# Performance work log

Measured on AMD Instinct MI355X. Metric: run time of the kernel, lower is better.

The kernel has to match this reference:

```python
import jax, jax.numpy as jnp
import numpy as np

S, B, V, E, H, L, HM = 256, 16, 20000, 512, 256, 2, 128  # seq, batch, vocab, emb, hidden, layers, mlp hidden
THRESH = 0.5


def setup_inputs() -> dict:
    key = jax.random.key(0)
    ks = jax.random.split(key, 8)
    sc = 0.05
    concepts = jax.random.randint(ks[0], (S, B), 0, V)
    concepts_lengths = jnp.full((B,), S, dtype=jnp.int32)  # full-length sequences
    emb = jax.random.normal(ks[1], (V, E), jnp.float32) * sc
    # stacked PyTorch-style LSTM weights: [layer, direction(0=fwd,1=bwd), 4H, in]
    w_ih = jax.random.normal(ks[2], (L, 2, 4 * H, E), jnp.float32) * sc
    w_hh = jax.random.normal(ks[3], (L, 2, 4 * H, H), jnp.float32) * sc
    b = jax.random.normal(ks[4], (L, 2, 4 * H), jnp.float32) * sc  # b_ih + b_hh combined
    Ua = jax.random.normal(ks[5], (HM, 2 * H), jnp.float32) * sc
    Wa = jax.random.normal(ks[6], (HM, 2 * H), jnp.float32) * sc
    va = jax.random.normal(ks[7], (1, HM), jnp.float32) * sc
    return dict(concepts=concepts, concepts_lengths=concepts_lengths, emb=emb,
                w_ih=w_ih, w_hh=w_hh, b=b, Ua=Ua, Wa=Wa, va=va)


def _lstm_dir(x, wi, wh, bb, reverse):
    # x: [S, B, in]; PyTorch gate order i, f, g, o
    h0 = jnp.zeros((x.shape[1], H), x.dtype)

    def step(carry, xt):
        h, c = carry
        g = xt @ wi.T + h @ wh.T + bb  # [B, 4H]
        i, f, gg, o = jnp.split(g, 4, axis=-1)
        c = jax.nn.sigmoid(f) * c + jax.nn.sigmoid(i) * jnp.tanh(gg)
        h = jax.nn.sigmoid(o) * jnp.tanh(c)
        return (h, c), h

    _, hs = jax.lax.scan(step, (h0, h0), x, reverse=reverse)
    return hs  # [S, B, H]


def reference(concepts, concepts_lengths, emb, w_ih, w_hh, b, Ua, Wa, va):
    x = emb[concepts]  # [S, B, E]
    for l in range(L):  # fixed small layer count
        f = _lstm_dir(x, w_ih[l, 0], w_hh[l, 0], b[l, 0], False)
        r = _lstm_dir(x, w_ih[l, 1], w_hh[l, 1], b[l, 1], True)
        x = jnp.concatenate([f, r], axis=-1)  # [S, B, 2H]
    enc = x.transpose(1, 0, 2)  # [B, S, 2H]
    p = enc @ Ua.T  # [B, S, HM]  Ua(parent)
    c = enc @ Wa.T  # [B, S, HM]  Wa(child)
    # fused pairwise: va(tanh(Ua(p_i) + Wa(c_j))) -> [B, S, S]
    scores = jnp.einsum('bijh,h->bij', jnp.tanh(p[:, :, None, :] + c[:, None, :, :]), va[0])
    predictions = (jax.nn.sigmoid(scores) >= THRESH).astype(jnp.int32)
    return scores, predictions
```

## Files before the change

kernel.cpp:

```cpp
#include <hip/hip_runtime.h>


#define S_    256
#define B_    16
#define E_    512
#define H_    256
#define HM_   128
#define M_    4096

typedef __attribute__((ext_vector_type(8))) short short8;
typedef __attribute__((ext_vector_type(4))) float f32x4;
union u32x4s8 { unsigned int u[4]; uint4 u4; short8 v; };

__device__ __forceinline__ float sigm(float x) { return 1.f / (1.f + __expf(-x)); }
__device__ __forceinline__ float tanh_fast(float x) {
  x = fminf(fmaxf(x, -15.f), 15.f);
  float e = __expf(2.f * x);
  return (e - 1.f) / (e + 1.f);
}
__device__ __forceinline__ unsigned short f2bf(float f) {
  unsigned u = __float_as_uint(f);
  u += 0x7FFFu + ((u >> 16) & 1u);
  return (unsigned short)(u >> 16);
}
__device__ __forceinline__ float bf2f(unsigned short s) {
  return __uint_as_float(((unsigned)s) << 16);
}
__device__ __forceinline__ unsigned int packsplit(float f) {
  unsigned short m = f2bf(f);
  unsigned short r = f2bf(f - bf2f(m));
  return (unsigned)m | ((unsigned)r << 16);
}

__global__ void k_gather_pk(const int* __restrict__ concepts, const float* __restrict__ emb,
                            unsigned int* __restrict__ Xpk) {
  int m = blockIdx.x;
  int tok = concepts[m];
  const float4* src = reinterpret_cast<const float4*>(emb + (size_t)tok * E_);
  uint4* dst = reinterpret_cast<uint4*>(Xpk + (size_t)m * E_);
  for (int i = threadIdx.x; i < E_ / 4; i += blockDim.x) {
    float4 v = src[i];
    uint4 o;
    o.x = packsplit(v.x); o.y = packsplit(v.y); o.z = packsplit(v.z); o.w = packsplit(v.w);
    dst[i] = o;
  }
}

__global__ void k_pack(const float* __restrict__ in, unsigned int* __restrict__ out, int n4) {
  int i = blockIdx.x * blockDim.x + threadIdx.x;
  if (i < n4) {
    float4 v = reinterpret_cast<const float4*>(in)[i];
    uint4 o;
    o.x = packsplit(v.x); o.y = packsplit(v.y); o.z = packsplit(v.z); o.w = packsplit(v.w);
    reinterpret_cast<uint4*>(out)[i] = o;
  }
}

__global__ __launch_bounds__(256) void k_gemm_pk(const unsigned int* __restrict__ Apk,
                                                 const unsigned int* __restrict__ Wpk,
                                                 const float* __restrict__ bias,
                                                 float* __restrict__ C, int N, int K) {
  __shared__ unsigned int As[128][36];
  __shared__ unsigned int Ws2[128][36];
  const int bm = blockIdx.x * 128, bn = blockIdx.y * 128;
  const int tid = threadIdx.x;
  const int wave = tid >> 6, lane = tid & 63;
  const int wm = (wave >> 1) << 6, wn = (wave & 1) << 6;
  const int l16 = lane & 15, quad = lane >> 4;
  const int r = tid >> 1, cb = (tid & 1) << 4;

  f32x4 acc[4][4];
#pragma unroll
  for (int i = 0; i < 4; ++i)
#pragma unroll
    for (int j = 0; j < 4; ++j) acc[i][j] = (f32x4){0.f, 0.f, 0.f, 0.f};

  for (int k0 = 0; k0 < K; k0 += 32) {
    const unsigned int* pa = Apk + (size_t)(bm + r) * K + k0 + cb;
    const unsigned int* pw = Wpk + (size_t)(bn + r) * K + k0 + cb;
    uint4 a0 = *(const uint4*)pa, a1 = *(const uint4*)(pa + 4),
          a2 = *(const uint4*)(pa + 8), a3 = *(const uint4*)(pa + 12);
    uint4 w0 = *(const uint4*)pw, w1 = *(const uint4*)(pw + 4),
          w2 = *(const uint4*)(pw + 8), w3 = *(const uint4*)(pw + 12);
    __syncthreads();
    *(uint4*)&As[r][cb] = a0;  *(uint4*)&As[r][cb + 4] = a1;
    *(uint4*)&As[r][cb + 8] = a2; *(uint4*)&As[r][cb + 12] = a3;
    *(uint4*)&Ws2[r][cb] = w0; *(uint4*)&Ws2[r][cb + 4] = w1;
    *(uint4*)&Ws2[r][cb + 8] = w2; *(uint4*)&Ws2[r][cb + 12] = w3;
    __syncthreads();

    short8 Amv[4], Arv[4], Bmv[4], Brv[4];
#pragma unroll
    for (int t = 0; t < 4; ++t) {
      const unsigned int* p = &As[wm + (t << 4) + l16][quad << 3];
      uint4 p0 = *(const uint4*)p, p1 = *(const uint4*)(p + 4);
      u32x4s8 m, rr;
      m.u[0] = __builtin_amdgcn_perm(p0.y, p0.x, 0x05040100u);
      rr.u[0] = __builtin_amdgcn_perm(p0.y, p0.x, 0x07060302u);
      m.u[1] = __builtin_amdgcn_perm(p0.w, p0.z, 0x05040100u);
      rr.u[1] = __builtin_amdgcn_perm(p0.w, p0.z, 0x07060302u);
      m.u[2] = __builtin_amdgcn_perm(p1.y, p1.x, 0x05040100u);
      rr.u[2] = __builtin_amdgcn_perm(p1.y, p1.x, 0x07060302u);
      m.u[3] = __builtin_amdgcn_perm(p1.w, p1.z, 0x05040100u);
      rr.u[3] = __builtin_amdgcn_perm(p1.w, p1.z, 0x07060302u);
      Amv[t] = m.v; Arv[t] = rr.v;
      const unsigned int* pb = &Ws2[wn + (t << 4) + l16][quad << 3];
      uint4 q0 = *(const uint4*)pb, q1 = *(const uint4*)(pb + 4);
      m.u[0] = __builtin_amdgcn_perm(q0.y, q0.x, 0x05040100u);
      rr.u[0] = __builtin_amdgcn_perm(q0.y, q0.x, 0x07060302u);
      m.u[1] = __builtin_amdgcn_perm(q0.w, q0.z, 0x05040100u);
      rr.u[1] = __builtin_amdgcn_perm(q0.w, q0.z, 0x07060302u);
      m.u[2] = __builtin_amdgcn_perm(q1.y, q1.x, 0x05040100u);
      rr.u[2] = __builtin_amdgcn_perm(q1.y, q1.x, 0x07060302u);
      m.u[3] = __builtin_amdgcn_perm(q1.w, q1.z, 0x05040100u);
      rr.u[3] = __builtin_amdgcn_perm(q1.w, q1.z, 0x07060302u);
      Bmv[t] = m.v; Brv[t] = rr.v;
    }
#pragma unroll
    for (int ti = 0; ti < 4; ++ti)
#pragma unroll
      for (int tj = 0; tj < 4; ++tj) {
        acc[ti][tj] = __builtin_amdgcn_mfma_f32_16x16x32_bf16(Amv[ti], Bmv[tj], acc[ti][tj], 0, 0, 0);
        acc[ti][tj] = __builtin_amdgcn_mfma_f32_16x16x32_bf16(Amv[ti], Brv[tj], acc[ti][tj], 0, 0, 0);
        acc[ti][tj] = __builtin_amdgcn_mfma_f32_16x16x32_bf16(Arv[ti], Bmv[tj], acc[ti][tj], 0, 0, 0);
      }
  }

  float bv[4];
#pragma unroll
  for (int tj = 0; tj < 4; ++tj)
    bv[tj] = bias ? bias[bn + wn + (tj << 4) + l16] : 0.f;
#pragma unroll
  for (int ti = 0; ti < 4; ++ti)
#pragma unroll
    for (int rr = 0; rr < 4; ++rr) {
      float* crow = C + (size_t)(bm + wm + (ti << 4) + (quad << 2) + rr) * N + bn + wn + l16;
      crow[0]  = acc[ti][0][rr] + bv[0];
      crow[16] = acc[ti][1][rr] + bv[1];
      crow[32] = acc[ti][2][rr] + bv[2];
      crow[48] = acc[ti][3][rr] + bv[3];
    }
}

__global__ __launch_bounds__(256) void k_gemm(const float* __restrict__ A,
                                              const float* __restrict__ W,
                                              const float* __restrict__ bias,
                                              float* __restrict__ C,
                                              int M, int N, int K) {
  __shared__ __align__(16) float As[16][132];
  __shared__ __align__(16) float Ws[16][132];
  const int bm = blockIdx.x * 128, bn = blockIdx.y * 128;
  const int tid = threadIdx.x;
  const int tm = (tid >> 4) * 8, tn = (tid & 15) * 8;
  float acc[8][8];
#pragma unroll
  for (int i = 0; i < 8; i++)
#pragma unroll
    for (int j = 0; j < 8; j++) acc[i][j] = 0.f;

  const int lr = tid >> 1, lk = (tid & 1) * 8;
  for (int k0 = 0; k0 < K; k0 += 16) {
    float4 a0 = *(const float4*)(A + (size_t)(bm + lr) * K + k0 + lk);
    float4 a1 = *(const float4*)(A + (size_t)(bm + lr) * K + k0 + lk + 4);
    float4 w0 = *(const float4*)(W + (size_t)(bn + lr) * K + k0 + lk);
    float4 w1 = *(const float4*)(W + (size_t)(bn + lr) * K + k0 + lk + 4);
    As[lk + 0][lr] = a0.x; As[lk + 1][lr] = a0.y; As[lk + 2][lr] = a0.z; As[lk + 3][lr] = a0.w;
    As[lk + 4][lr] = a1.x; As[lk + 5][lr] = a1.y; As[lk + 6][lr] = a1.z; As[lk + 7][lr] = a1.w;
    Ws[lk + 0][lr] = w0.x; Ws[lk + 1][lr] = w0.y; Ws[lk + 2][lr] = w0.z; Ws[lk + 3][lr] = w0.w;
    Ws[lk + 4][lr] = w1.x; Ws[lk + 5][lr] = w1.y; Ws[lk + 6][lr] = w1.z; Ws[lk + 7][lr] = w1.w;
    __syncthreads();
#pragma unroll
    for (int k = 0; k < 16; k++) {
      float4 av0 = *(const float4*)&As[k][tm];
      float4 av1 = *(const float4*)&As[k][tm + 4];
      float4 wv0 = *(const float4*)&Ws[k][tn];
      float4 wv1 = *(const float4*)&Ws[k][tn + 4];
      float a[8] = {av0.x, av0.y, av0.z, av0.w, av1.x, av1.y, av1.z, av1.w};
      float w[8] = {wv0.x, wv0.y, wv0.z, wv0.w, wv1.x, wv1.y, wv1.z, wv1.w};
#pragma unroll
      for (int i = 0; i < 8; i++)
#pragma unroll
        for (int j = 0; j < 8; j++) acc[i][j] += a[i] * w[j];
    }
    __syncthreads();
  }

  float bv[8];
#pragma unroll
  for (int j = 0; j < 8; j++) bv[j] = bias ? bias[bn + tn + j] : 0.f;
#pragma unroll
  for (int i = 0; i < 8; i++) {
    float4 v0 = make_float4(acc[i][0] + bv[0], acc[i][1] + bv[1], acc[i][2] + bv[2], acc[i][3] + bv[3]);
    float4 v1 = make_float4(acc[i][4] + bv[4], acc[i][5] + bv[5], acc[i][6] + bv[6], acc[i][7] + bv[7]);
    *(float4*)(C + (size_t)(bm + tm + i) * N + bn + tn) = v0;
    *(float4*)(C + (size_t)(bm + tm + i) * N + bn + tn + 4) = v1;
  }
}

__global__ __launch_bounds__(512) void k_lstm(const float* __restrict__ Gin,
                                              const float* __restrict__ whh,
                                              float* __restrict__ Houtf,
                                              unsigned int* __restrict__ Houtp,
                                              unsigned long long* __restrict__ Hbuf) {
  const int d = blockIdx.x >> 4;
  const int g = blockIdx.x & 15;
  const int tid = threadIdx.x;
  const int w8 = tid >> 6;
  const int lane = tid & 63;
  const int bcol = lane & 15;
  const int quad = lane >> 4;
  const int u_e = tid & 15;
  const int b_e = (tid >> 4) & 15;
  const int ws = (w8 + g) & 7;
  __shared__ unsigned int hL[16 * 260];
  __shared__ __align__(16) float Lg[4][16][24];

  unsigned int Am[8][4], Ar[8][4];
  if (w8 < 4) {
    const float* wrow = whh + (size_t)((d << 10) + (w8 << 8) + (g << 4) + bcol) * 256;
#pragma unroll
    for (int s = 0; s < 8; ++s) {
      float w[8];
      *(float4*)&w[0] = *(const float4*)(wrow + s * 32 + quad * 8);
      *(float4*)&w[4] = *(const float4*)(wrow + s * 32 + quad * 8 + 4);
#pragma unroll
      for (int j = 0; j < 4; ++j) {
        unsigned short m0 = f2bf(w[2 * j]), m1 = f2bf(w[2 * j + 1]);
        unsigned short r0 = f2bf(w[2 * j] - bf2f(m0));
        unsigned short r1 = f2bf(w[2 * j + 1] - bf2f(m1));
        Am[s][j] = (unsigned)m0 | ((unsigned)m1 << 16);
        Ar[s][j] = (unsigned)r0 | ((unsigned)r1 << 16);
      }
    }
  }

  float c_reg = 0.f;
  for (int it = 0; it < 256; ++it) {
    const int step = d ? (255 - it) : it;

    float gin[4];
    if (tid < 256) {
#pragma unroll
      for (int qq = 0; qq < 4; ++qq)
        gin[qq] = Gin[((size_t)((step << 4) + b_e) << 11) + (d << 10) + (qq << 8) + (g << 4) + u_e];
    }

    if (it > 0) {
      const unsigned long long* src = Hbuf + ((size_t)((d << 1) + ((it - 1) & 1)) << 12);
      const unsigned long long* p0 = src + (ws << 9) + lane;
      const unsigned int want = (unsigned int)it;
      unsigned long long v[8];
#pragma unroll
      for (int c = 0; c < 8; ++c)
        v[c] = __hip_atomic_load(p0 + (c << 6), __ATOMIC_RELAXED, __HIP_MEMORY_SCOPE_AGENT);
      for (;;) {
        unsigned int badm = 0;
#pragma unroll
        for (int c = 0; c < 8; ++c)
          badm |= ((unsigned int)(v[c] >> 32) != want) ? (1u << c) : 0u;
        if (__ballot(badm != 0) == 0ull) break;
#pragma unroll
        for (int c = 0; c < 8; ++c)
          if (badm & (1u << c))
            v[c] = __hip_atomic_load(p0 + (c << 6), __ATOMIC_RELAXED, __HIP_MEMORY_SCOPE_AGENT);
      }
#pragma unroll
      for (int c = 0; c < 8; ++c) {
        int e_b = (ws << 1) + (c >> 2);
        int e_k = ((c & 3) << 6) + lane;
        hL[e_b * 260 + e_k] = (unsigned int)v[c];
      }
    }
    __syncthreads();

    if (w8 < 4) {
      f32x4 acc0 = {0.f, 0.f, 0.f, 0.f}, acc1 = acc0, acc2 = acc0;
      if (it > 0) {
#pragma unroll
        for (int s = 0; s < 8; ++s) {
          const unsigned int* p = &hL[bcol * 260 + (s << 5) + (quad << 3)];
          uint4 p0v = *(const uint4*)p;
          uint4 p1v = *(const uint4*)(p + 4);
          u32x4s8 Bm, Br, Amu, Aru;
          Bm.u[0] = __builtin_amdgcn_perm(p0v.y, p0v.x, 0x05040100u);
          Br.u[0] = __builtin_amdgcn_perm(p0v.y, p0v.x, 0x07060302u);
          Bm.u[1] = __builtin_amdgcn_perm(p0v.w, p0v.z, 0x05040100u);
          Br.u[1] = __builtin_amdgcn_perm(p0v.w, p0v.z, 0x07060302u);
          Bm.u[2] = __builtin_amdgcn_perm(p1v.y, p1v.x, 0x05040100u);
          Br.u[2] = __builtin_amdgcn_perm(p1v.y, p1v.x, 0x07060302u);
          Bm.u[3] = __builtin_amdgcn_perm(p1v.w, p1v.z, 0x05040100u);
          Br.u[3] = __builtin_amdgcn_perm(p1v.w, p1v.z, 0x07060302u);
#pragma unroll
          for (int j = 0; j < 4; ++j) { Amu.u[j] = Am[s][j]; Aru.u[j] = Ar[s][j]; }
          acc0 = __builtin_amdgcn_mfma_f32_16x16x32_bf16(Amu.v, Bm.v, acc0, 0, 0, 0);
          acc1 = __builtin_amdgcn_mfma_f32_16x16x32_bf16(Amu.v, Br.v, acc1, 0, 0, 0);
          acc2 = __builtin_amdgcn_mfma_f32_16x16x32_bf16(Aru.v, Bm.v, acc2, 0, 0, 0);
        }
      }
      f32x4 t = acc0 + acc1 + acc2;
      *(float4*)&Lg[w8][bcol][quad << 2] = make_float4(t[0], t[1], t[2], t[3]);
    }
    __syncthreads();

    if (tid < 256) {
      float gi = Lg[0][b_e][u_e] + gin[0];
      float gf = Lg[1][b_e][u_e] + gin[1];
      float gg = Lg[2][b_e][u_e] + gin[2];
      float go = Lg[3][b_e][u_e] + gin[3];
      float ct = sigm(gf) * c_reg + sigm(gi) * tanh_fast(gg);
      c_reg = ct;
      float h = sigm(go) * tanh_fast(ct);
      unsigned short hm = f2bf(h);
      unsigned short hr = f2bf(h - bf2f(hm));
      unsigned int hpk = ((unsigned)hr << 16) | (unsigned)hm;
      unsigned long long hp = ((unsigned long long)(unsigned int)(it + 1) << 32) |
                              (unsigned long long)hpk;
      __hip_atomic_store(Hbuf + ((size_t)((d << 1) + (it & 1)) << 12) + (b_e << 8) + (g << 4) + u_e,
                         hp, __ATOMIC_RELAXED, __HIP_MEMORY_SCOPE_AGENT);
      size_t oidx = (size_t)((step << 4) + b_e) * 512 + (d << 8) + (g << 4) + u_e;
      Houtf[oidx] = h;
      Houtp[oidx] = hpk;
    }
  }
}

__global__ __launch_bounds__(256) void k_attn(const float* __restrict__ P,
                                              const float* __restrict__ Cc,
                                              const float* __restrict__ va,
                                              float* __restrict__ out) {
  const int b = blockIdx.x & 15, i = blockIdx.x >> 4;
  __shared__ float pv[128], vv[128];
  const int t = threadIdx.x;
  if (t < 128) {
    pv[t] = P[(size_t)((i << 4) + b) * 128 + t];
    vv[t] = va[t];
  }
  __syncthreads();
  const float4* c4 = reinterpret_cast<const float4*>(Cc + (size_t)((t << 4) + b) * 128);
  float acc = 0.f;
#pragma unroll 8
  for (int hh = 0; hh < 32; ++hh) {
    float4 cv = c4[hh];
    int h = hh << 2;
    acc += vv[h]     * tanh_fast(pv[h]     + cv.x);
    acc += vv[h + 1] * tanh_fast(pv[h + 1] + cv.y);
    acc += vv[h + 2] * tanh_fast(pv[h + 2] + cv.z);
    acc += vv[h + 3] * tanh_fast(pv[h + 3] + cv.w);
  }
  size_t o = ((size_t)b << 16) + ((size_t)i << 8) + (size_t)t;
  out[o] = acc;
  out[(1u << 20) + o] = (acc >= 0.f) ? 1.f : 0.f;
}

extern "C" void kernel_launch(void* const* d_in, const int* in_sizes, int n_in,
                              void* d_out, int out_size, void* d_ws, size_t ws_size,
                              hipStream_t stream) {
  const int*   concepts = (const int*)d_in[0];
  const float* emb  = (const float*)d_in[2];
  const float* w_ih = (const float*)d_in[3];
  const float* w_hh = (const float*)d_in[4];
  const float* bias = (const float*)d_in[5];
  const float* Ua   = (const float*)d_in[6];
  const float* Wa   = (const float*)d_in[7];
  const float* va   = (const float*)d_in[8];
  float* out = (float*)d_out;
  float* ws  = (float*)d_ws;

  constexpr size_t OFF_G   = 0;
  constexpr size_t OFF_PK  = OFF_G  + (size_t)M_ * 2048;
  constexpr size_t OFF_WPK = OFF_PK + (size_t)M_ * 512;
  constexpr size_t OFF_HF  = OFF_WPK + 2 * 2048 * 512;
  constexpr size_t OFF_P   = OFF_HF + (size_t)M_ * 512;
  constexpr size_t OFF_C   = OFF_P  + (size_t)M_ * HM_;
  constexpr size_t OFF_HB  = OFF_C  + (size_t)M_ * HM_;

  float* G  = ws + OFF_G;
  unsigned int* PK  = (unsigned int*)(ws + OFF_PK);
  unsigned int* WPK = (unsigned int*)(ws + OFF_WPK);
  float* HF = ws + OFF_HF;
  float* Pm = ws + OFF_P;
  float* Cm = ws + OFF_C;
  unsigned long long* Hb0 = (unsigned long long*)(ws + OFF_HB);
  unsigned long long* Hb1 = Hb0 + 2 * 2 * 4096;

  k_pack<<<(2 * 2048 * 512 / 4 + 255) / 256, 256, 0, stream>>>(w_ih, WPK, 2 * 2048 * 512 / 4);
  k_gather_pk<<<M_, 128, 0, stream>>>(concepts, emb, PK);

  k_gemm_pk<<<dim3(32, 16), 256, 0, stream>>>(PK, WPK, bias, G, 2048, 512);
  k_lstm<<<32, 512, 0, stream>>>(G, w_hh, HF, PK, Hb0);

  k_gemm_pk<<<dim3(32, 16), 256, 0, stream>>>(PK, WPK + (size_t)2048 * 512, bias + 2048,
                                              G, 2048, 512);
  k_lstm<<<32, 512, 0, stream>>>(G, w_hh + (size_t)2048 * 256, HF, PK, Hb1);

  k_gemm<<<dim3(32, 1), 256, 0, stream>>>(HF, Ua, nullptr, Pm, M_, HM_, 512);
  k_gemm<<<dim3(32, 1), 256, 0, stream>>>(HF, Wa, nullptr, Cm, M_, HM_, 512);

  k_attn<<<M_, 256, 0, stream>>>(Pm, Cm, va, out);
}
```

Before: 1.551 ms.

## Interleave gate rows so each LSTM lane owns a unit, dropping one barrier per step

The recurrent weight rows are permuted so each MFMA output lane holds all four gates (i, f, g, o) for one hidden unit. The cell update now runs directly in registers, which removes the Lg shared staging buffer and one __syncthreads per timestep. The input-gate GEMM output is transposed to a gate-major layout to match the new per-lane gate reads. Hidden-state polling now uses inline-asm dwordx4 loads with sc1 into a double-buffered LDS region. The cost is tighter coupling of layouts across kernels, and the inline-asm loads depend on the cache bit giving the needed coherence.

```diff
diff --git a/kernel.cpp b/kernel.cpp
--- a/kernel.cpp
+++ b/kernel.cpp
@@ -10,6 +10,7 @@
 
 typedef __attribute__((ext_vector_type(8))) short short8;
 typedef __attribute__((ext_vector_type(4))) float f32x4;
+typedef __attribute__((ext_vector_type(4))) unsigned int u32x4v;
 union u32x4s8 { unsigned int u[4]; uint4 u4; short8 v; };
 
 __device__ __forceinline__ float sigm(float x) { return 1.f / (1.f + __expf(-x)); }
@@ -30,6 +31,24 @@
   unsigned short m = f2bf(f);
   unsigned short r = f2bf(f - bf2f(m));
   return (unsigned)m | ((unsigned)r << 16);
+}
+
+__device__ __forceinline__ void stage4_sc1(u32x4v v[4], const u32x4v* p) {
+  asm volatile(
+      "global_load_dwordx4 %0, %4, off sc1\n\t"
+      "global_load_dwordx4 %1, %4, off offset:1024 sc1\n\t"
+      "global_load_dwordx4 %2, %4, off offset:2048 sc1\n\t"
+      "global_load_dwordx4 %3, %4, off offset:3072 sc1\n\t"
+      "s_waitcnt vmcnt(0)"
+      : "=&v"(v[0]), "=&v"(v[1]), "=&v"(v[2]), "=&v"(v[3])
+      : "v"(p)
+      : "memory");
+}
+__device__ __forceinline__ u32x4v stage1_sc1(const u32x4v* p) {
+  u32x4v r;
+  asm volatile("global_load_dwordx4 %0, %1, off sc1\n\ts_waitcnt vmcnt(0)"
+               : "=v"(r) : "v"(p) : "memory");
+  return r;
 }
 
 __global__ void k_gather_pk(const int* __restrict__ concepts, const float* __restrict__ emb,
@@ -59,7 +78,7 @@
 __global__ __launch_bounds__(256) void k_gemm_pk(const unsigned int* __restrict__ Apk,
                                                  const unsigned int* __restrict__ Wpk,
                                                  const float* __restrict__ bias,
-                                                 float* __restrict__ C, int N, int K) {
+                                                 float* __restrict__ C, int K) {
   __shared__ unsigned int As[128][36];
   __shared__ unsigned int Ws2[128][36];
   const int bm = blockIdx.x * 128, bn = blockIdx.y * 128;
@@ -126,25 +145,21 @@
       }
   }
 
-  float bv[4];
-#pragma unroll
-  for (int tj = 0; tj < 4; ++tj)
-    bv[tj] = bias ? bias[bn + wn + (tj << 4) + l16] : 0.f;
-#pragma unroll
-  for (int ti = 0; ti < 4; ++ti)
-#pragma unroll
-    for (int rr = 0; rr < 4; ++rr) {
-      float* crow = C + (size_t)(bm + wm + (ti << 4) + (quad << 2) + rr) * N + bn + wn + l16;
-      crow[0]  = acc[ti][0][rr] + bv[0];
-      crow[16] = acc[ti][1][rr] + bv[1];
-      crow[32] = acc[ti][2][rr] + bv[2];
-      crow[48] = acc[ti][3][rr] + bv[3];
-    }
+#pragma unroll
+  for (int tj = 0; tj < 4; ++tj) {
+    float bv = bias ? bias[bn + wn + (tj << 4) + l16] : 0.f;
+#pragma unroll
+    for (int ti = 0; ti < 4; ++ti) {
+      float4 vv = make_float4(acc[ti][tj][0] + bv, acc[ti][tj][1] + bv,
+                              acc[ti][tj][2] + bv, acc[ti][tj][3] + bv);
+      *(float4*)(C + (size_t)(bn + wn + (tj << 4) + l16) * 4096 +
+                 bm + wm + (ti << 4) + (quad << 2)) = vv;
+    }
+  }
 }
 
 __global__ __launch_bounds__(256) void k_gemm(const float* __restrict__ A,
                                               const float* __restrict__ W,
-                                              const float* __restrict__ bias,
                                               float* __restrict__ C,
                                               int M, int N, int K) {
   __shared__ __align__(16) float As[16][132];
@@ -184,14 +199,10 @@
     }
     __syncthreads();
   }
-
-  float bv[8];
-#pragma unroll
-  for (int j = 0; j < 8; j++) bv[j] = bias ? bias[bn + tn + j] : 0.f;
 #pragma unroll
   for (int i = 0; i < 8; i++) {
-    float4 v0 = make_float4(acc[i][0] + bv[0], acc[i][1] + bv[1], acc[i][2] + bv[2], acc[i][3] + bv[3]);
-    float4 v1 = make_float4(acc[i][4] + bv[4], acc[i][5] + bv[5], acc[i][6] + bv[6], acc[i][7] + bv[7]);
+    float4 v0 = make_float4(acc[i][0], acc[i][1], acc[i][2], acc[i][3]);
+    float4 v1 = make_float4(acc[i][4], acc[i][5], acc[i][6], acc[i][7]);
     *(float4*)(C + (size_t)(bm + tm + i) * N + bn + tn) = v0;
     *(float4*)(C + (size_t)(bm + tm + i) * N + bn + tn + 4) = v1;
   }
@@ -209,15 +220,13 @@
   const int lane = tid & 63;
   const int bcol = lane & 15;
   const int quad = lane >> 4;
-  const int u_e = tid & 15;
-  const int b_e = (tid >> 4) & 15;
   const int ws = (w8 + g) & 7;
-  __shared__ unsigned int hL[16 * 260];
-  __shared__ __align__(16) float Lg[4][16][24];
+  __shared__ __align__(16) unsigned int hL[2 * 4160];
 
   unsigned int Am[8][4], Ar[8][4];
   if (w8 < 4) {
-    const float* wrow = whh + (size_t)((d << 10) + (w8 << 8) + (g << 4) + bcol) * 256;
+    const int unit = (g << 4) + (w8 << 2) + (bcol >> 2);
+    const float* wrow = whh + (size_t)((d << 10) + ((bcol & 3) << 8) + unit) * 256;
 #pragma unroll
     for (int s = 0; s < 8; ++s) {
       float w[8];
@@ -234,51 +243,53 @@
     }
   }
 
+  const int unit_e = (g << 4) + (w8 << 2) + quad;
   float c_reg = 0.f;
   for (int it = 0; it < 256; ++it) {
     const int step = d ? (255 - it) : it;
 
-    float gin[4];
-    if (tid < 256) {
-#pragma unroll
-      for (int qq = 0; qq < 4; ++qq)
-        gin[qq] = Gin[((size_t)((step << 4) + b_e) << 11) + (d << 10) + (qq << 8) + (g << 4) + u_e];
-    }
-
     if (it > 0) {
-      const unsigned long long* src = Hbuf + ((size_t)((d << 1) + ((it - 1) & 1)) << 12);
-      const unsigned long long* p0 = src + (ws << 9) + lane;
+      const u32x4v* src =
+          (const u32x4v*)(Hbuf + ((size_t)((d << 1) + ((it - 1) & 1)) << 12));
+      const u32x4v* p0 = src + (ws << 8) + lane;
       const unsigned int want = (unsigned int)it;
-      unsigned long long v[8];
-#pragma unroll
-      for (int c = 0; c < 8; ++c)
-        v[c] = __hip_atomic_load(p0 + (c << 6), __ATOMIC_RELAXED, __HIP_MEMORY_SCOPE_AGENT);
+      u32x4v v[4];
+      stage4_sc1(v, p0);
       for (;;) {
         unsigned int badm = 0;
 #pragma unroll
-        for (int c = 0; c < 8; ++c)
-          badm |= ((unsigned int)(v[c] >> 32) != want) ? (1u << c) : 0u;
+        for (int c = 0; c < 4; ++c)
+          badm |= ((v[c].y != want) | (v[c].w != want)) ? (1u << c) : 0u;
         if (__ballot(badm != 0) == 0ull) break;
 #pragma unroll
-        for (int c = 0; c < 8; ++c)
-          if (badm & (1u << c))
-            v[c] = __hip_atomic_load(p0 + (c << 6), __ATOMIC_RELAXED, __HIP_MEMORY_SCOPE_AGENT);
+        for (int c = 0; c < 4; ++c)
+          if (badm & (1u << c)) v[c] = stage1_sc1(p0 + (c << 6));
       }
-#pragma unroll
-      for (int c = 0; c < 8; ++c) {
-        int e_b = (ws << 1) + (c >> 2);
-        int e_k = ((c & 3) << 6) + lane;
-        hL[e_b * 260 + e_k] = (unsigned int)v[c];
+      unsigned int* dL = &hL[(it & 1) * 4160];
+#pragma unroll
+      for (int c = 0; c < 4; ++c) {
+        int b = (ws << 1) + (c >> 1);
+        int k = ((c & 1) << 7) + (lane << 1);
+        *(unsigned long long*)&dL[b * 260 + k] =
+            (unsigned long long)v[c].x | ((unsigned long long)v[c].z << 32);
       }
+    }
+
+    float gin[4];
+    if (w8 < 4) {
+#pragma unroll
+      for (int gate = 0; gate < 4; ++gate)
+        gin[gate] = Gin[((size_t)((d << 10) + (gate << 8) + unit_e) << 12) + (step << 4) + bcol];
     }
     __syncthreads();
 
     if (w8 < 4) {
       f32x4 acc0 = {0.f, 0.f, 0.f, 0.f}, acc1 = acc0, acc2 = acc0;
       if (it > 0) {
+        const unsigned int* hb = &hL[(it & 1) * 4160];
 #pragma unroll
         for (int s = 0; s < 8; ++s) {
-          const unsigned int* p = &hL[bcol * 260 + (s << 5) + (quad << 3)];
+          const unsigned int* p = &hb[bcol * 260 + (s << 5) + (quad << 3)];
           uint4 p0v = *(const uint4*)p;
           uint4 p1v = *(const uint4*)(p + 4);
           u32x4s8 Bm, Br, Amu, Aru;
@@ -298,26 +309,17 @@
         }
       }
       f32x4 t = acc0 + acc1 + acc2;
-      *(float4*)&Lg[w8][bcol][quad << 2] = make_float4(t[0], t[1], t[2], t[3]);
-    }
-    __syncthreads();
-
-    if (tid < 256) {
-      float gi = Lg[0][b_e][u_e] + gin[0];
-      float gf = Lg[1][b_e][u_e] + gin[1];
-      float gg = Lg[2][b_e][u_e] + gin[2];
-      float go = Lg[3][b_e][u_e] + gin[3];
-      float ct = sigm(gf) * c_reg + sigm(gi) * tanh_fast(gg);
+      float ct = sigm(t[1] + gin[1]) * c_reg + sigm(t[0] + gin[0]) * tanh_fast(t[2] + gin[2]);
       c_reg = ct;
-      float h = sigm(go) * tanh_fast(ct);
+      float h = sigm(t[3] + gin[3]) * tanh_fast(ct);
       unsigned short hm = f2bf(h);
       unsigned short hr = f2bf(h - bf2f(hm));
       unsigned int hpk = ((unsigned)hr << 16) | (unsigned)hm;
       unsigned long long hp = ((unsigned long long)(unsigned int)(it + 1) << 32) |
                               (unsigned long long)hpk;
-      __hip_atomic_store(Hbuf + ((size_t)((d << 1) + (it & 1)) << 12) + (b_e << 8) + (g << 4) + u_e,
+      __hip_atomic_store(Hbuf + ((size_t)((d << 1) + (it & 1)) << 12) + (bcol << 8) + unit_e,
                          hp, __ATOMIC_RELAXED, __HIP_MEMORY_SCOPE_AGENT);
-      size_t oidx = (size_t)((step << 4) + b_e) * 512 + (d << 8) + (g << 4) + u_e;
+      size_t oidx = (size_t)((step << 4) + bcol) * 512 + (d << 8) + unit_e;
       Houtf[oidx] = h;
       Houtp[oidx] = hpk;
     }
@@ -386,15 +388,14 @@
   k_pack<<<(2 * 2048 * 512 / 4 + 255) / 256, 256, 0, stream>>>(w_ih, WPK, 2 * 2048 * 512 / 4);
   k_gather_pk<<<M_, 128, 0, stream>>>(concepts, emb, PK);
 
-  k_gemm_pk<<<dim3(32, 16), 256, 0, stream>>>(PK, WPK, bias, G, 2048, 512);
+  k_gemm_pk<<<dim3(32, 16), 256, 0, stream>>>(PK, WPK, bias, G, 512);
   k_lstm<<<32, 512, 0, stream>>>(G, w_hh, HF, PK, Hb0);
 
-  k_gemm_pk<<<dim3(32, 16), 256, 0, stream>>>(PK, WPK + (size_t)2048 * 512, bias + 2048,
-                                              G, 2048, 512);
+  k_gemm_pk<<<dim3(32, 16), 256, 0, stream>>>(PK, WPK + (size_t)2048 * 512, bias + 2048, G, 512);
   k_lstm<<<32, 512, 0, stream>>>(G, w_hh + (size_t)2048 * 256, HF, PK, Hb1);
 
-  k_gemm<<<dim3(32, 1), 256, 0, stream>>>(HF, Ua, nullptr, Pm, M_, HM_, 512);
-  k_gemm<<<dim3(32, 1), 256, 0, stream>>>(HF, Wa, nullptr, Cm, M_, HM_, 512);
+  k_gemm<<<dim3(32, 1), 256, 0, stream>>>(HF, Ua, Pm, M_, HM_, 512);
+  k_gemm<<<dim3(32, 1), 256, 0, stream>>>(HF, Wa, Cm, M_, HM_, 512);
 
   k_attn<<<M_, 256, 0, stream>>>(Pm, Cm, va, out);
 }
```

After: 1.997 ms. 28.8% more time.
